# Optimization experiments

Hardware: AMD Instinct MI355X
Metric: run time of the kernel (lower is better)

The kernel has to match this reference:

```python
import jax, jax.numpy as jnp
import numpy as np

SEQ_LEN = 4096
D_MODEL = 1024
OUT_DIM = 1024
KERNEL = 256
STRIDE = 16
NUM_HEADS = 16


def _p(key, *shape):
    return jax.random.normal(key, shape, dtype=jnp.float32) * 0.02


def setup_inputs() -> dict:
    key = jax.random.key(0)
    ks = jax.random.split(key, 12)
    return {
        "path": jax.random.normal(ks[0], (SEQ_LEN, D_MODEL), dtype=jnp.float32),
        # sliding_module (nn.MultiheadAttention, embed_dim=D_MODEL)
        "w_in1": _p(ks[1], 3 * D_MODEL, D_MODEL),
        "b_in1": jnp.zeros((3 * D_MODEL,), jnp.float32),
        "w_out1": _p(ks[2], D_MODEL, D_MODEL),
        "b_out1": jnp.zeros((D_MODEL,), jnp.float32),
        # linear_module
        "w_lin": _p(ks[3], OUT_DIM, D_MODEL),
        "b_lin": jnp.zeros((OUT_DIM,), jnp.float32),
        # accum_module (embed_dim=OUT_DIM)
        "w_in2": _p(ks[4], 3 * OUT_DIM, OUT_DIM),
        "b_in2": jnp.zeros((3 * OUT_DIM,), jnp.float32),
        "w_out2": _p(ks[5], OUT_DIM, OUT_DIM),
        "b_out2": jnp.zeros((OUT_DIM,), jnp.float32),
    }


def _mha(q, k, v, w_in, b_in, w_out, b_out, num_heads):
    """torch nn.MultiheadAttention math (dropout=0). q,k,v: [..., L, E]."""
    E = q.shape[-1]
    Dh = E // num_heads
    wq, wk, wv = jnp.split(w_in, 3, axis=0)
    bq, bk, bv = jnp.split(b_in, 3)
    def heads(t):
        return t.reshape(t.shape[:-1] + (num_heads, Dh))
    qh = heads(q @ wq.T + bq)
    kh = heads(k @ wk.T + bk)
    vh = heads(v @ wv.T + bv)
    scale = 1.0 / np.sqrt(Dh).astype(np.float32)
    att = jax.nn.softmax(jnp.einsum("...qhd,...khd->...hqk", qh, kh) * scale, axis=-1)
    out = jnp.einsum("...hqk,...khd->...qhd", att, vh)
    out = out.reshape(out.shape[:-2] + (E,))
    return out @ w_out.T + b_out


def reference(path, w_in1, b_in1, w_out1, b_out1, w_lin, b_lin,
              w_in2, b_in2, w_out2, b_out2):
    seq_len = path.shape[-2]
    slices_num = (seq_len - KERNEL) // STRIDE
    # overlapping windows: [slices_num, KERNEL, D_MODEL]
    idx = jnp.arange(slices_num)[:, None] * STRIDE + jnp.arange(KERNEL)[None, :]
    x = path[idx]
    # batched self-attention over windows
    x = _mha(x, x, x, w_in1, b_in1, w_out1, b_out1, NUM_HEADS)
    x = jax.nn.relu(x @ w_lin.T + b_lin)  # [slices_num, KERNEL, OUT_DIM]
    # sequential recurrent attention accumulation
    def step(cum_att, xi):
        new = _mha(xi, cum_att, cum_att, w_in2, b_in2, w_out2, b_out2, NUM_HEADS)
        return new, None
    cum_att, _ = jax.lax.scan(step, x[0], x[1:])
    return cum_att  # [KERNEL, OUT_DIM]
```

## Files before the change

kernel.cpp:

```cpp
#include <hip/hip_runtime.h>
#include <math.h>

#define D_MODEL 1024
#define N_WIN   240
#define TOK     256
#define NH      16
#define DH      64
#define CHUNK   8
#define NCHUNK  30
#define WIN     ((size_t)TOK * D_MODEL)

typedef unsigned short ushort_t;
typedef unsigned long long ull_t;
typedef __attribute__((ext_vector_type(8))) short short8;
typedef __attribute__((ext_vector_type(4))) float floatx4;

__device__ __forceinline__ ushort_t f2bf(float f) {
    unsigned u = __float_as_uint(f);
    unsigned lsb = (u >> 16) & 1u;
    u += 0x7fffu + lsb;
    return (ushort_t)(u >> 16);
}

__device__ __forceinline__ void st2_wt(ushort_t* p, ushort_t v) {
    unsigned vv = v;
    asm volatile("global_store_short %0, %1, off sc1"
                 :: "v"(p), "v"(vv) : "memory");
}
__device__ __forceinline__ void st8_wt(ushort_t* p, ushort4 v) {
    ull_t dv = (ull_t)((unsigned)v.x | ((unsigned)v.y << 16))
             | ((ull_t)((unsigned)v.z | ((unsigned)v.w << 16)) << 32);
    asm volatile("global_store_dwordx2 %0, %1, off sc1"
                 :: "v"(p), "v"(dv) : "memory");
}
__device__ __forceinline__ void rel_drain() {
    asm volatile("s_waitcnt vmcnt(0)" ::: "memory");
}

#define GLDS(g, l) __builtin_amdgcn_global_load_lds( \
    (const __attribute__((address_space(1))) unsigned int*)(g), \
    (__attribute__((address_space(3))) unsigned int*)(l), 16, 0, 0)

__device__ __forceinline__ void grid_bar(unsigned* base, int g, unsigned s)
{
    rel_drain();
    __syncthreads();
    if (threadIdx.x == 0) {
        unsigned old = __hip_atomic_fetch_add(base + g * 32, 1u,
                __ATOMIC_RELAXED, __HIP_MEMORY_SCOPE_AGENT);
        if (old == 8u * s - 1u) {
            unsigned r = __hip_atomic_fetch_add(base + 256, 1u,
                    __ATOMIC_RELAXED, __HIP_MEMORY_SCOPE_AGENT);
            if (r == 8u * s - 1u)
                __hip_atomic_store(base + 288, s, __ATOMIC_RELAXED,
                                   __HIP_MEMORY_SCOPE_AGENT);
        }
        while (__hip_atomic_load(base + 288, __ATOMIC_RELAXED,
                                 __HIP_MEMORY_SCOPE_AGENT) < s)
            __builtin_amdgcn_s_sleep(1);
    }
    __syncthreads();
}

__device__ __forceinline__ void help_bar(unsigned* base, int g, unsigned s)
{
    rel_drain();
    __syncthreads();
    if (threadIdx.x == 0) {
        unsigned old = __hip_atomic_fetch_add(base + 1024 + g * 32, 1u,
                __ATOMIC_RELAXED, __HIP_MEMORY_SCOPE_AGENT);
        if (old == 8u * s - 1u) {
            unsigned r = __hip_atomic_fetch_add(base + 1800, 1u,
                    __ATOMIC_RELAXED, __HIP_MEMORY_SCOPE_AGENT);
            if (r == 24u * s - 1u)
                __hip_atomic_store(base + 1832, s, __ATOMIC_RELAXED,
                                   __HIP_MEMORY_SCOPE_AGENT);
        }
        while (__hip_atomic_load(base + 1832, __ATOMIC_RELAXED,
                                 __HIP_MEMORY_SCOPE_AGENT) < s)
            __builtin_amdgcn_s_sleep(1);
    }
    __syncthreads();
}

__global__ __launch_bounds__(256) void cast_bf_k(
    const float* __restrict__ s, ushort_t* __restrict__ d, int n)
{
    int i = (blockIdx.x * 256 + threadIdx.x) * 4;
    if (i >= n) return;
    float4 v = *(const float4*)(s + i);
    ushort4 o;
    o.x = f2bf(v.x); o.y = f2bf(v.y); o.z = f2bf(v.z); o.w = f2bf(v.w);
    *(ushort4*)(d + i) = o;
}

__global__ __launch_bounds__(256) void transpose_k(
    const ushort_t* __restrict__ src, ushort_t* __restrict__ dst)
{
    __shared__ ushort_t t[64][65];
    const int bx = blockIdx.x * 64, by = blockIdx.y * 64;
    const int c = threadIdx.x & 63, r0 = threadIdx.x >> 6;
#pragma unroll
    for (int k = 0; k < 16; ++k) {
        int r = r0 + k * 4;
        t[r][c] = src[(size_t)(by + r) * 1024 + bx + c];
    }
    __syncthreads();
#pragma unroll
    for (int k = 0; k < 16; ++k) {
        int r = r0 + k * 4;
        dst[(size_t)(bx + r) * 1024 + by + c] = t[c][r];
    }
}

__global__ __launch_bounds__(256) void bc_k(
    const float* __restrict__ w_in2, const float* __restrict__ b_in2,
    const float* __restrict__ b_out2, float* __restrict__ bc)
{
    int n = blockIdx.x * 256 + threadIdx.x;
    const float* row = w_in2 + (size_t)(1024 + n) * 1024;
    float s = b_in2[1024 + n];
    for (int j = 0; j < 1024; j += 4) {
        float4 w = *(const float4*)(row + j);
        float4 b = *(const float4*)(b_out2 + j);
        s += w.x * b.x + w.y * b.y + w.z * b.z + w.w * b.w;
    }
    bc[n] = s;
}

template<bool GATHER, bool WT>
__device__ __forceinline__ void gemm_core(
    ushort_t* As, ushort_t* Bs,
    const ushort_t* __restrict__ A, int lda, int w0,
    const ushort_t* __restrict__ W, const float* __restrict__ bias,
    ushort_t* __restrict__ Cb, float* __restrict__ Cf, int ldc,
    int K, int m0, int n0, int co, int relu)
{
    const int tid = threadIdx.x;
    const int wave = tid >> 6, lane = tid & 63;
    const int wm = wave & 1, wn = wave >> 1;

    int r0 = m0 + (tid >> 2), r1 = r0 + 64;
    if (GATHER) {
        r0 = (w0 + (r0 >> 8)) * 16 + (r0 & 255);
        r1 = (w0 + (r1 >> 8)) * 16 + (r1 & 255);
    }
    const int kcol = (tid & 3) * 8;
    const ushort_t* gA0 = A + (size_t)r0 * lda + kcol;
    const ushort_t* gA1 = A + (size_t)r1 * lda + kcol;
    const ushort_t* pW  = W + (size_t)n0 * K;
    const ushort_t* gB0 = pW + (size_t)(tid >> 2) * K + kcol;
    const ushort_t* gB1 = gB0 + (size_t)64 * K;
    ushort_t* lA = As + wave * 512;
    ushort_t* lB = Bs + wave * 512;

    floatx4 acc[4][4];
#pragma unroll
    for (int i = 0; i < 4; ++i)
#pragma unroll
        for (int j = 0; j < 4; ++j) acc[i][j] = (floatx4){0.f, 0.f, 0.f, 0.f};

    const int fr = lane & 15, fk = (lane >> 4) * 8;
    const int arow = (wm * 64 + fr) * 32 + fk;
    const int brow = (wn * 64 + fr) * 32 + fk;

    for (int k0 = 0; k0 < K; k0 += 32) {
        GLDS(gA0 + k0, lA);
        GLDS(gA1 + k0, lA + 2048);
        GLDS(gB0 + k0, lB);
        GLDS(gB1 + k0, lB + 2048);
        __syncthreads();
        short8 a[4], b[4];
#pragma unroll
        for (int mi = 0; mi < 4; ++mi) a[mi] = *(const short8*)&As[arow + mi * 512];
#pragma unroll
        for (int ni = 0; ni < 4; ++ni) b[ni] = *(const short8*)&Bs[brow + ni * 512];
#pragma unroll
        for (int mi = 0; mi < 4; ++mi)
#pragma unroll
            for (int ni = 0; ni < 4; ++ni)
                acc[mi][ni] = __builtin_amdgcn_mfma_f32_16x16x32_bf16(
                    a[mi], b[ni], acc[mi][ni], 0, 0, 0);
        __syncthreads();
    }

    const int crq = (lane >> 4) * 4;
    const int ccol = lane & 15;
#pragma unroll
    for (int mi = 0; mi < 4; ++mi) {
#pragma unroll
        for (int ni = 0; ni < 4; ++ni) {
            int lc = wn * 64 + ni * 16 + ccol;
            float bz = bias[n0 + lc];
#pragma unroll
            for (int rg = 0; rg < 4; ++rg) {
                int row = m0 + wm * 64 + mi * 16 + crq + rg;
                float v = acc[mi][ni][rg] + bz;
                if (relu) v = fmaxf(v, 0.f);
                size_t off = (size_t)row * ldc + co + lc;
                if (Cb) {
                    if (WT) st2_wt(Cb + off, f2bf(v));
                    else    Cb[off] = f2bf(v);
                }
                if (Cf) Cf[off] = v;
            }
        }
    }
}

__global__ __launch_bounds__(256) void gemm_bf_k(
    const ushort_t* __restrict__ A, int lda,
    const ushort_t* __restrict__ W, const float* __restrict__ bias,
    ushort_t* __restrict__ Cb, float* __restrict__ Cf, int ldc,
    int K, int relu)
{
    __shared__ ushort_t As[128 * 32];
    __shared__ ushort_t Bs[128 * 32];
    gemm_core<false, false>(As, Bs, A, lda, 0, W, bias, Cb, Cf, ldc, K,
                            blockIdx.y * 128, blockIdx.x * 128, blockIdx.x * 128, relu);
}

__global__ __launch_bounds__(256) void gemm_qkv_k(
    const ushort_t* __restrict__ path_bf, const ushort_t* __restrict__ W,
    const float* __restrict__ bias, ushort_t* __restrict__ Cb, int w0)
{
    __shared__ ushort_t As[128 * 32];
    __shared__ ushort_t Bs[128 * 32];
    gemm_core<true, false>(As, Bs, path_bf, 1024, w0, W, bias, Cb, nullptr, 3072, 1024,
                           blockIdx.y * 128, blockIdx.x * 128, blockIdx.x * 128, 0);
}

#define PLD 260
#define VLD 132

struct AttnShared {
    ushort_t P[64 * PLD];
    ushort_t VT[64 * VLD];
    float    l[64];
};

__device__ void attn_body(AttnShared& sh,
    const ushort_t* __restrict__ qkv, ushort_t* __restrict__ ao,
    int rs, int h, int b)
{
    const ushort_t* base = qkv + (size_t)b * TOK * 3072;
    const ushort_t* Q = base;
    const ushort_t* K = base + 1024;
    const ushort_t* V = base + 2048;
    ushort_t* O = ao + (size_t)b * TOK * 1024;
    const int ldq = 3072, ldkv = 3072, ldo = 1024;
    const int tid = threadIdx.x;
    const int wave = tid >> 6, lane = tid & 63;
    const int fr = lane & 15, q = lane >> 4, fk = q * 8;
    const ushort_t* Qh = Q + (size_t)(rs * 64) * ldq + h * 64;
    const ushort_t* Kh = K + h * 64;
    const ushort_t* Vh = V + h * 64;
    const int m0 = wave * 16;

    floatx4 s[16];
#pragma unroll
    for (int nt = 0; nt < 16; ++nt) s[nt] = (floatx4){0.f, 0.f, 0.f, 0.f};
#pragma unroll
    for (int kc = 0; kc < 64; kc += 32) {
        short8 a = *(const short8*)(Qh + (size_t)(m0 + fr) * ldq + kc + fk);
#pragma unroll
        for (int nt = 0; nt < 16; ++nt) {
            short8 b2 = *(const short8*)(Kh + (size_t)(nt * 16 + fr) * ldkv + kc + fk);
            s[nt] = __builtin_amdgcn_mfma_f32_16x16x32_bf16(a, b2, s[nt], 0, 0, 0);
        }
    }

    float rmax[4] = {-INFINITY, -INFINITY, -INFINITY, -INFINITY};
#pragma unroll
    for (int nt = 0; nt < 16; ++nt)
#pragma unroll
        for (int rg = 0; rg < 4; ++rg) rmax[rg] = fmaxf(rmax[rg], s[nt][rg]);
#pragma unroll
    for (int d = 1; d < 16; d <<= 1)
#pragma unroll
        for (int rg = 0; rg < 4; ++rg)
            rmax[rg] = fmaxf(rmax[rg], __shfl_xor(rmax[rg], d));

    float rsum[4] = {0.f, 0.f, 0.f, 0.f};
#pragma unroll
    for (int nt = 0; nt < 16; ++nt) {
#pragma unroll
        for (int rg = 0; rg < 4; ++rg) {
            float p = __expf((s[nt][rg] - rmax[rg]) * 0.125f);
            rsum[rg] += p;
            sh.P[(m0 + q * 4 + rg) * PLD + nt * 16 + fr] = f2bf(p);
        }
    }
#pragma unroll
    for (int d = 1; d < 16; d <<= 1)
#pragma unroll
        for (int rg = 0; rg < 4; ++rg) rsum[rg] += __shfl_xor(rsum[rg], d);
    if (fr == 0) {
#pragma unroll
        for (int rg = 0; rg < 4; ++rg) sh.l[m0 + q * 4 + rg] = rsum[rg];
    }
    __syncthreads();

    floatx4 o[4];
#pragma unroll
    for (int i = 0; i < 4; ++i) o[i] = (floatx4){0.f, 0.f, 0.f, 0.f};

#pragma unroll
    for (int half = 0; half < 2; ++half) {
        {
            int r = tid & 127, cp = tid >> 7;
            const ushort_t* vrow = Vh + (size_t)(half * 128 + r) * ldkv + cp * 32;
#pragma unroll
            for (int c = 0; c < 4; ++c) {
                uint4 pk = *(const uint4*)(vrow + c * 8);
                int d0 = cp * 32 + c * 8;
                sh.VT[(d0 + 0) * VLD + r] = (ushort_t)(pk.x & 0xffff);
                sh.VT[(d0 + 1) * VLD + r] = (ushort_t)(pk.x >> 16);
                sh.VT[(d0 + 2) * VLD + r] = (ushort_t)(pk.y & 0xffff);
                sh.VT[(d0 + 3) * VLD + r] = (ushort_t)(pk.y >> 16);
                sh.VT[(d0 + 4) * VLD + r] = (ushort_t)(pk.z & 0xffff);
                sh.VT[(d0 + 5) * VLD + r] = (ushort_t)(pk.z >> 16);
                sh.VT[(d0 + 6) * VLD + r] = (ushort_t)(pk.w & 0xffff);
                sh.VT[(d0 + 7) * VLD + r] = (ushort_t)(pk.w >> 16);
            }
        }
        __syncthreads();
#pragma unroll
        for (int ks = 0; ks < 4; ++ks) {
            short8 a = *(const short8*)&sh.P[(m0 + fr) * PLD + half * 128 + ks * 32 + fk];
#pragma unroll
            for (int nt2 = 0; nt2 < 4; ++nt2) {
                short8 b2 = *(const short8*)&sh.VT[(nt2 * 16 + fr) * VLD + ks * 32 + fk];
                o[nt2] = __builtin_amdgcn_mfma_f32_16x16x32_bf16(a, b2, o[nt2], 0, 0, 0);
            }
        }
        __syncthreads();
    }

    float linv[4];
#pragma unroll
    for (int rg = 0; rg < 4; ++rg) linv[rg] = 1.f / sh.l[m0 + q * 4 + rg];
#pragma unroll
    for (int nt2 = 0; nt2 < 4; ++nt2)
#pragma unroll
        for (int rg = 0; rg < 4; ++rg) {
            int row = rs * 64 + m0 + q * 4 + rg;
            st2_wt(O + (size_t)row * ldo + h * 64 + nt2 * 16 + fr,
                   f2bf(o[nt2][rg] * linv[rg]));
        }
    __syncthreads();
}

__global__ __launch_bounds__(256) void attn_mfma_k(
    const ushort_t* __restrict__ qkv, ushort_t* __restrict__ ao)
{
    __shared__ AttnShared sh;
    attn_body(sh, qkv, ao, blockIdx.x, blockIdx.y, blockIdx.z);
}

#define KLD 76
#define TLD 264

struct ScanSmem {
    union {
        struct { ushort_t Ab[2][4096]; ushort_t Wb[3][8192]; } st;
        struct { ushort_t Kl[256 * KLD]; ushort_t Vt[64 * TLD];
                 ushort_t P[64 * TLD]; } at;
    };
};

__device__ __forceinline__ void stage_A(
    const ushort_t* __restrict__ A64, int k0, ushort_t* __restrict__ Ad,
    int wave, int lane)
{
#pragma unroll
    for (int t = 0; t < 2; ++t) {
        int j = wave * 128 + t * 64 + lane;
        int row = j >> 3;
        int blk = (j & 7) ^ (row & 7);
        GLDS(A64 + (size_t)row * 1024 + k0 + blk * 8,
             Ad + wave * 1024 + t * 512);
    }
}

__device__ __forceinline__ void stage_W(
    const ushort_t* __restrict__ Wsel, int h, int k0,
    ushort_t* __restrict__ Wd, int wave, int lane)
{
#pragma unroll
    for (int t = 0; t < 4; ++t) {
        int j = wave * 256 + t * 64 + lane;
        int r = j >> 3;
        int blk = (j & 7) ^ (r & 7);
        int n = ((r >> 6) << 10) + h * 64 + (r & 63);
        GLDS(Wsel + (size_t)n * 1024 + k0 + blk * 8,
             Wd + wave * 2048 + t * 512);
    }
}

__device__ void scan_body(
    ScanSmem& sm, int h, int rs, int g,
    const ushort_t* __restrict__ Qchunk, int i0, int w0, int nsteps,
    const ushort_t* __restrict__ x0, ushort_t* __restrict__ AOb,
    ushort_t* __restrict__ KVx,
    const ushort_t* __restrict__ Wkv, const float* __restrict__ bkv,
    const ushort_t* __restrict__ Wc, const float* __restrict__ bc,
    unsigned* __restrict__ bar, unsigned s0)
{
    const int tid = threadIdx.x;
    const int wave = tid >> 6, lane = tid & 63;
    const int fr = lane & 15, q = lane >> 4, fk = q * 8;
    const int m0g = rs * 64 + wave * 16;

    const int dbofs = (wave < 2 ? 0 : 1024) + h * 64 + (wave & 1) * 32;
    float bK1[2], bC1[2];
#pragma unroll
    for (int nt = 0; nt < 2; ++nt) {
        bK1[nt] = bkv[dbofs + nt * 16 + fr];
        bC1[nt] = bc[dbofs + nt * 16 + fr];
    }

    ushort_t* Kl = sm.at.Kl;
    ushort_t* Vt = sm.at.Vt;
    ushort_t* P  = sm.at.P;

    short8 qf0, qf1;
    {
        const int i = i0;
        const ushort_t* Wsel0 = (i == 1) ? Wkv : Wc;
        stage_W(Wsel0, h, 0,  sm.st.Wb[0], wave, lane);
        stage_W(Wsel0, h, 64, sm.st.Wb[1], wave, lane);
        const ushort_t* Qrow = Qchunk + (size_t)(i - w0) * WIN
            + (size_t)(m0g + fr) * 1024 + h * 64;
        qf0 = *(const short8*)(Qrow);
        qf1 = *(const short8*)(Qrow + 32);
        const ushort_t* Asrc0 = (i == 1) ? x0
            : AOb + (size_t)((i - 1) & 7) * WIN;
        stage_A(Asrc0 + (size_t)rs * 64 * 1024, 0, sm.st.Ab[0], wave, lane);
    }

    unsigned s = s0;
    for (int t0 = 0; t0 < nsteps; ++t0, ++s) {
        const int i = i0 + t0;
        const ushort_t* Asrc = (i == 1) ? x0
            : AOb + (size_t)((i - 1) & 7) * WIN;
        const ushort_t* Wsel = (i == 1) ? Wkv : Wc;
        const ushort_t* A64 = Asrc + (size_t)rs * 64 * 1024;
        ushort_t* KVs = KVx + (size_t)(i & 7) * (NH * 32768) + h * 32768;

        floatx4 acc[4][2];
#pragma unroll
        for (int mt = 0; mt < 4; ++mt)
#pragma unroll
            for (int nt = 0; nt < 2; ++nt)
                acc[mt][nt] = (floatx4){0.f, 0.f, 0.f, 0.f};

#pragma unroll 1
        for (int t = 0; t < 16; ++t) {
            if (t < 15)
                stage_A(A64, (t + 1) * 64, sm.st.Ab[(t + 1) & 1], wave, lane);
            if (t < 14)
                stage_W(Wsel, h, (t + 2) * 64, sm.st.Wb[(t + 2) % 3], wave, lane);
            if (t == 15)
                asm volatile("s_waitcnt vmcnt(0)" ::: "memory");
            else if (t == 0 || t == 14)
                asm volatile("s_waitcnt vmcnt(6)" ::: "memory");
            else
                asm volatile("s_waitcnt vmcnt(10)" ::: "memory");
            __builtin_amdgcn_s_barrier();
            const ushort_t* Ac  = sm.st.Ab[t & 1];
            const ushort_t* Wc_ = sm.st.Wb[t % 3];
#pragma unroll
            for (int kh = 0; kh < 2; ++kh) {
                const int pb = (((kh << 2) + q) ^ (fr & 7)) * 8;
                short8 a[4];
#pragma unroll
                for (int mt = 0; mt < 4; ++mt)
                    a[mt] = *(const short8*)&Ac[(mt * 16 + fr) * 64 + pb];
#pragma unroll
                for (int nt = 0; nt < 2; ++nt) {
                    short8 b = *(const short8*)
                        &Wc_[(wave * 32 + nt * 16 + fr) * 64 + pb];
#pragma unroll
                    for (int mt = 0; mt < 4; ++mt)
                        acc[mt][nt] = __builtin_amdgcn_mfma_f32_16x16x32_bf16(
                            a[mt], b, acc[mt][nt], 0, 0, 0);
                }
            }
            asm volatile("s_waitcnt lgkmcnt(0)" ::: "memory");
            __builtin_amdgcn_sched_barrier(0);
            __builtin_amdgcn_s_barrier();
        }

        ushort_t* Kx = KVs;
        ushort_t* Vx = KVs + 16384;
#pragma unroll
        for (int mt = 0; mt < 4; ++mt) {
#pragma unroll
            for (int nt = 0; nt < 2; ++nt) {
                const float bz = (i == 1) ? bK1[nt] : bC1[nt];
                const int d = (wave & 1) * 32 + nt * 16 + fr;
                if (wave < 2) {
#pragma unroll
                    for (int rg = 0; rg < 4; ++rg) {
                        const int key = rs * 64 + mt * 16 + q * 4 + rg;
                        st2_wt(Kx + key * 64 + d, f2bf(acc[mt][nt][rg] + bz));
                    }
                } else {
                    ushort4 pv;
                    pv.x = f2bf(acc[mt][nt][0] + bz);
                    pv.y = f2bf(acc[mt][nt][1] + bz);
                    pv.z = f2bf(acc[mt][nt][2] + bz);
                    pv.w = f2bf(acc[mt][nt][3] + bz);
                    st8_wt(Vx + d * 256 + rs * 64 + mt * 16 + q * 4, pv);
                }
            }
        }
        rel_drain();
        __syncthreads();
        if (tid == 0)
            __hip_atomic_fetch_add(bar + 384 + h * 32, 1u,
                    __ATOMIC_RELAXED, __HIP_MEMORY_SCOPE_AGENT);

#pragma unroll
        for (int mt = 0; mt < 4; ++mt) {
#pragma unroll
            for (int nt = 0; nt < 2; ++nt) {
                const float bz = (i == 1) ? bK1[nt] : bC1[nt];
                const int d = (wave & 1) * 32 + nt * 16 + fr;
                if (wave < 2) {
#pragma unroll
                    for (int rg = 0; rg < 4; ++rg) {
                        const int key = rs * 64 + mt * 16 + q * 4 + rg;
                        Kl[key * KLD + d] = f2bf(acc[mt][nt][rg] + bz);
                    }
                } else {
                    ushort4 pv;
                    pv.x = f2bf(acc[mt][nt][0] + bz);
                    pv.y = f2bf(acc[mt][nt][1] + bz);
                    pv.z = f2bf(acc[mt][nt][2] + bz);
                    pv.w = f2bf(acc[mt][nt][3] + bz);
                    *(ushort4*)&Vt[d * TLD + rs * 64 + mt * 16 + q * 4] = pv;
                }
            }
        }
        if (tid == 0) {
            while (__hip_atomic_load(bar + 384 + h * 32, __ATOMIC_RELAXED,
                                     __HIP_MEMORY_SCOPE_AGENT) < 4u * s)
                __builtin_amdgcn_s_sleep(1);
        }
        __syncthreads();

        {
            if (wave != rs) {
                const ushort_t* kr = Kx + tid * 64;
                uint4 kb4[8];
#pragma unroll
                for (int s8 = 0; s8 < 8; ++s8)
                    kb4[s8] = *(const uint4*)(kr + s8 * 8);
                const int kp = (tid >> 4) & 3;
#pragma unroll
                for (int s8 = 0; s8 < 8; ++s8) {
                    int ks = (s8 + kp) & 7;
                    *(uint4*)&Kl[tid * KLD + ks * 8] = kb4[ks];
                }
            }
            const int vd = tid >> 2, vq = tid & 3;
            if (vq != rs) {
                const ushort_t* vr = Vx + vd * 256 + vq * 64;
                uint4 vb4[8];
#pragma unroll
                for (int s8 = 0; s8 < 8; ++s8)
                    vb4[s8] = *(const uint4*)(vr + s8 * 8);
                const int vp = vq << 1;
#pragma unroll
                for (int s8 = 0; s8 < 8; ++s8) {
                    int vs = (s8 + vp) & 7;
                    *(uint4*)&Vt[vd * TLD + vq * 64 + vs * 8] = vb4[vs];
                }
            }
        }
        __syncthreads();

        ushort_t* AOcur = AOb + (size_t)(i & 7) * WIN;
        {
            const int pl0 = wave * 16;
            floatx4 sc[16];
#pragma unroll
            for (int nt = 0; nt < 16; ++nt) sc[nt] = (floatx4){0.f, 0.f, 0.f, 0.f};
#pragma unroll
            for (int kc = 0; kc < 64; kc += 32) {
                short8 a = (kc == 0) ? qf0 : qf1;
#pragma unroll
                for (int nt = 0; nt < 16; ++nt) {
                    short8 b = *(const short8*)&Kl[(nt * 16 + fr) * KLD + kc + fk];
                    sc[nt] = __builtin_amdgcn_mfma_f32_16x16x32_bf16(
                        a, b, sc[nt], 0, 0, 0);
                }
            }
            float rmax[4] = {-INFINITY, -INFINITY, -INFINITY, -INFINITY};
#pragma unroll
            for (int nt = 0; nt < 16; ++nt)
#pragma unroll
                for (int rg = 0; rg < 4; ++rg) rmax[rg] = fmaxf(rmax[rg], sc[nt][rg]);
#pragma unroll
            for (int d = 1; d < 16; d <<= 1)
#pragma unroll
                for (int rg = 0; rg < 4; ++rg)
                    rmax[rg] = fmaxf(rmax[rg], __shfl_xor(rmax[rg], d));
            float rsum[4] = {0.f, 0.f, 0.f, 0.f};
#pragma unroll
            for (int nt = 0; nt < 16; ++nt) {
#pragma unroll
                for (int rg = 0; rg < 4; ++rg) {
                    float p = __expf((sc[nt][rg] - rmax[rg]) * 0.125f);
                    rsum[rg] += p;
                    P[(pl0 + q * 4 + rg) * TLD + nt * 16 + fr] = f2bf(p);
                }
            }
#pragma unroll
            for (int d = 1; d < 16; d <<= 1)
#pragma unroll
                for (int rg = 0; rg < 4; ++rg) rsum[rg] += __shfl_xor(rsum[rg], d);

            floatx4 o[4];
#pragma unroll
            for (int nt = 0; nt < 4; ++nt) o[nt] = (floatx4){0.f, 0.f, 0.f, 0.f};
#pragma unroll
            for (int kt = 0; kt < 8; ++kt) {
                short8 a = *(const short8*)&P[(pl0 + fr) * TLD + kt * 32 + fk];
#pragma unroll
                for (int nt = 0; nt < 4; ++nt) {
                    short8 b = *(const short8*)&Vt[(nt * 16 + fr) * TLD + kt * 32 + fk];
                    o[nt] = __builtin_amdgcn_mfma_f32_16x16x32_bf16(
                        a, b, o[nt], 0, 0, 0);
                }
            }
            float linv[4];
#pragma unroll
            for (int rg = 0; rg < 4; ++rg) linv[rg] = 1.f / rsum[rg];
#pragma unroll
            for (int nt = 0; nt < 4; ++nt)
#pragma unroll
                for (int rg = 0; rg < 4; ++rg) {
                    int row = m0g + q * 4 + rg;
                    st2_wt(AOcur + (size_t)row * 1024 + h * 64 + nt * 16 + fr,
                           f2bf(o[nt][rg] * linv[rg]));
                }
        }

        rel_drain();
        __syncthreads();
        if (tid == 0) {
            unsigned old = __hip_atomic_fetch_add(bar + g * 32, 1u,
                    __ATOMIC_RELAXED, __HIP_MEMORY_SCOPE_AGENT);
            if (old == 8u * s - 1u) {
                unsigned r = __hip_atomic_fetch_add(bar + 256, 1u,
                        __ATOMIC_RELAXED, __HIP_MEMORY_SCOPE_AGENT);
                if (r == 8u * s - 1u)
                    __hip_atomic_store(bar + 288, s, __ATOMIC_RELAXED,
                                       __HIP_MEMORY_SCOPE_AGENT);
            }
        }
        const bool more = (t0 + 1 < nsteps);
        if (more) {
            stage_W(Wc, h, 0,  sm.st.Wb[0], wave, lane);
            stage_W(Wc, h, 64, sm.st.Wb[1], wave, lane);
            const ushort_t* Qrow = Qchunk + (size_t)(i + 1 - w0) * WIN
                + (size_t)(m0g + fr) * 1024 + h * 64;
            qf0 = *(const short8*)(Qrow);
            qf1 = *(const short8*)(Qrow + 32);
        }
        if (tid == 0) {
            while (__hip_atomic_load(bar + 288, __ATOMIC_RELAXED,
                                     __HIP_MEMORY_SCOPE_AGENT) < s)
                __builtin_amdgcn_s_sleep(1);
        }
        __syncthreads();
        if (more)
            stage_A(AOb + (size_t)(i & 7) * WIN + (size_t)rs * 64 * 1024, 0,
                    sm.st.Ab[0], wave, lane);
    }
}

struct GemmSmem { ushort_t As[128 * 32]; ushort_t Bs[128 * 32]; };
union FusedSmem { ScanSmem scan; GemmSmem gem; AttnShared att; };

__global__ __launch_bounds__(256, 1) void fused_k(
    const ushort_t* __restrict__ Qchunk, int i0, int w0, int nsteps,
    const ushort_t* __restrict__ x0, ushort_t* __restrict__ AOb,
    ushort_t* __restrict__ KVx,
    const ushort_t* __restrict__ Wkv, const float* __restrict__ bkv,
    const ushort_t* __restrict__ Wc, const float* __restrict__ bc,
    unsigned* __restrict__ bar, unsigned s0,
    int do_help, int w0n,
    const ushort_t* __restrict__ path_bf,
    const ushort_t* __restrict__ w_in1, const float* __restrict__ b_in1,
    ushort_t* __restrict__ qkv, ushort_t* __restrict__ ao,
    ushort_t* __restrict__ ybuf,
    const ushort_t* __restrict__ w_out1, const float* __restrict__ b_out1,
    const ushort_t* __restrict__ w_lin, const float* __restrict__ b_lin,
    ushort_t* __restrict__ Xc,
    const ushort_t* __restrict__ w_in2, const float* __restrict__ b_in2,
    ushort_t* __restrict__ Qnext, unsigned hs0)
{
    __shared__ FusedSmem sm;
    const int wg = blockIdx.x;
    const int x = wg & 7, y = wg >> 3;

    if (x < 2) {
        const int scanIdx = x * 32 + y;
        const int h  = (x << 3) | (y >> 2);
        const int rs = y & 3;
        const int g  = scanIdx & 7;
        scan_body(sm.scan, h, rs, g,
                  Qchunk, i0, w0, nsteps, x0, AOb, KVx,
                  Wkv, bkv, Wc, bc, bar, s0);
        return;
    }
    if (!do_help) return;

    const int hw = (x - 2) * 32 + y;
    const int hg = hw >> 3;

    for (int t = hw; t < 384; t += 192) {
        int bx = t % 24, by = t / 24;
        gemm_core<true, true>(sm.gem.As, sm.gem.Bs, path_bf, 1024, w0n,
                              w_in1, b_in1, qkv, nullptr, 3072, 1024,
                              by * 128, bx * 128, bx * 128, 0);
    }
    help_bar(bar, hg, hs0);

    for (int t = hw; t < 512; t += 192) {
        int rs = t & 3, h = (t >> 2) & 15, b = t >> 6;
        attn_body(sm.att, qkv, ao, rs, h, b);
    }
    help_bar(bar, hg, hs0 + 1);

    for (int t = hw; t < 128; t += 192) {
        int bx = t & 7, by = t >> 3;
        gemm_core<false, true>(sm.gem.As, sm.gem.Bs, ao, 1024, 0,
                               w_out1, b_out1, ybuf, nullptr, 1024, 1024,
                               by * 128, bx * 128, bx * 128, 0);
    }
    help_bar(bar, hg, hs0 + 2);

    for (int t = hw; t < 128; t += 192) {
        int bx = t & 7, by = t >> 3;
        gemm_core<false, true>(sm.gem.As, sm.gem.Bs, ybuf, 1024, 0,
                               w_lin, b_lin, Xc, nullptr, 1024, 1024,
                               by * 128, bx * 128, bx * 128, 1);
    }
    help_bar(bar, hg, hs0 + 3);

    for (int t = hw; t < 128; t += 192) {
        int bx = t & 7, by = t >> 3;
        gemm_core<false, true>(sm.gem.As, sm.gem.Bs, Xc, 1024, 0,
                               w_in2, b_in2, Qnext, nullptr, 1024, 1024,
                               by * 128, bx * 128, bx * 128, 0);
    }
}

extern "C" void kernel_launch(void* const* d_in, const int* in_sizes, int n_in,
                              void* d_out, int out_size, void* d_ws, size_t ws_size,
                              hipStream_t stream)
{
    const float* path   = (const float*)d_in[0];
    const float* w_in1  = (const float*)d_in[1];
    const float* b_in1  = (const float*)d_in[2];
    const float* w_out1 = (const float*)d_in[3];
    const float* b_out1 = (const float*)d_in[4];
    const float* w_lin  = (const float*)d_in[5];
    const float* b_lin  = (const float*)d_in[6];
    const float* w_in2  = (const float*)d_in[7];
    const float* b_in2  = (const float*)d_in[8];
    const float* w_out2 = (const float*)d_in[9];
    const float* b_out2 = (const float*)d_in[10];
    float* out = (float*)d_out;

    unsigned* bar = (unsigned*)d_ws;
    float* bc      = (float*)d_ws + 2048;
    float* zerosf  = bc + 2048;
    ushort_t* ws = (ushort_t*)d_ws + 16384;
    ushort_t* path_bf  = ws;
    ushort_t* w_in1_bf = path_bf  + (size_t)4096 * 1024;
    ushort_t* w_out1_bf= w_in1_bf + (size_t)3072 * 1024;
    ushort_t* w_lin_bf = w_out1_bf+ (size_t)1024 * 1024;
    ushort_t* w_in2_bf = w_lin_bf + (size_t)1024 * 1024;
    ushort_t* w_out2_bf= w_in2_bf + (size_t)3072 * 1024;
    ushort_t* WoT_bf   = w_out2_bf+ (size_t)1024 * 1024;
    ushort_t* Wc_bf    = WoT_bf   + (size_t)1024 * 1024;
    ushort_t* qkv_bf   = Wc_bf    + (size_t)2048 * 1024;
    ushort_t* ao_bf    = qkv_bf   + (size_t)2048 * 3072;
    ushort_t* ybuf_bf  = ao_bf    + (size_t)2048 * 1024;
    ushort_t* Xbuf     = ybuf_bf  + (size_t)2048 * 1024;
    ushort_t* Qb0      = Xbuf     + (size_t)2048 * 1024;
    ushort_t* Qb1      = Qb0      + (size_t)2048 * 1024;
    ushort_t* AOb      = Qb1      + (size_t)2048 * 1024;
    ushort_t* x0buf    = AOb + 8 * WIN;
    ushort_t* dummy    = x0buf + WIN;
    ushort_t* KVx      = dummy + WIN;
    ushort_t* Qb[2] = {Qb0, Qb1};

    hipMemsetAsync(bar, 0, 8192, stream);
    hipMemsetAsync(zerosf, 0, 1024 * sizeof(float), stream);

    cast_bf_k<<<4096, 256, 0, stream>>>(path,  path_bf,  4096 * 1024);
    cast_bf_k<<<3072, 256, 0, stream>>>(w_in1, w_in1_bf, 3072 * 1024);
    cast_bf_k<<<1024, 256, 0, stream>>>(w_out1, w_out1_bf, 1024 * 1024);
    cast_bf_k<<<1024, 256, 0, stream>>>(w_lin, w_lin_bf, 1024 * 1024);
    cast_bf_k<<<3072, 256, 0, stream>>>(w_in2, w_in2_bf, 3072 * 1024);
    cast_bf_k<<<1024, 256, 0, stream>>>(w_out2, w_out2_bf, 1024 * 1024);

    transpose_k<<<dim3(16, 16), 256, 0, stream>>>(w_out2_bf, WoT_bf);
    bc_k<<<8, 256, 0, stream>>>(w_in2, b_in2, b_out2, bc);
    gemm_bf_k<<<dim3(8, 16), 256, 0, stream>>>(
        w_in2_bf + (size_t)1024 * 1024, 1024, WoT_bf, zerosf,
        Wc_bf, nullptr, 1024, 1024, 0);

    gemm_qkv_k<<<dim3(24, 16), 256, 0, stream>>>(
        path_bf, w_in1_bf, b_in1, qkv_bf, 0);
    attn_mfma_k<<<dim3(4, NH, CHUNK), 256, 0, stream>>>(qkv_bf, ao_bf);
    gemm_bf_k<<<dim3(8, 16), 256, 0, stream>>>(
        ao_bf, 1024, w_out1_bf, b_out1, ybuf_bf, nullptr, 1024, 1024, 0);
    gemm_bf_k<<<dim3(8, 16), 256, 0, stream>>>(
        ybuf_bf, 1024, w_lin_bf, b_lin, Xbuf, nullptr, 1024, 1024, 1);
    gemm_bf_k<<<dim3(8, 16), 256, 0, stream>>>(
        Xbuf, 1024, w_in2_bf, b_in2, Qb[0], nullptr, 1024, 1024, 0);
    (void)hipMemcpyAsync(x0buf, Xbuf, WIN * sizeof(ushort_t),
                         hipMemcpyDeviceToDevice, stream);

    unsigned sbase = 1;
    for (int c = 0; c < NCHUNK; ++c) {
        int w0 = c * CHUNK;
        int i0 = (c == 0) ? 1 : w0;
        int nsteps = (c == 0) ? CHUNK - 1 : CHUNK;
        int do_help = (c + 1 < NCHUNK) ? 1 : 0;
        int w0n = (c + 1) * CHUNK;
        unsigned hs0 = (unsigned)(c * 4 + 1);
        const ushort_t* Qcur = Qb[c & 1];
        ushort_t* Qnext = Qb[(c + 1) & 1];
        const ushort_t* x0P = x0buf;
        ushort_t* AObP = AOb;
        ushort_t* KVxP = KVx;
        const ushort_t* WkvP = w_in2_bf + (size_t)1024 * 1024;
        const float* bkvP = b_in2 + 1024;
        const ushort_t* WcP = Wc_bf;
        const float* bcP = bc;
        unsigned* barP = bar;
        unsigned sb = sbase;
        const ushort_t* pathP = path_bf;
        const ushort_t* win1P = w_in1_bf;
        const float* bin1P = b_in1;
        ushort_t* qkvP = qkv_bf;
        ushort_t* aoP = ao_bf;
        ushort_t* ybufP = ybuf_bf;
        const ushort_t* wout1P = w_out1_bf;
        const float* bout1P = b_out1;
        const ushort_t* wlinP = w_lin_bf;
        const float* blinP = b_lin;
        ushort_t* XP = Xbuf;
        const ushort_t* win2P = w_in2_bf;
        const float* bin2P = b_in2;
        void* args[] = {&Qcur, &i0, &w0, &nsteps, &x0P, &AObP, &KVxP,
                        &WkvP, &bkvP, &WcP, &bcP, &barP, &sb,
                        &do_help, &w0n, &pathP, &win1P, &bin1P,
                        &qkvP, &aoP, &ybufP, &wout1P, &bout1P,
                        &wlinP, &blinP, &XP, &win2P, &bin2P, &Qnext, &hs0};
        hipLaunchCooperativeKernel((void*)fused_k, dim3(256), dim3(256),
                                   args, 0, stream);
        sbase += (unsigned)nsteps;
    }

    gemm_bf_k<<<dim3(8, 2), 256, 0, stream>>>(
        AOb + (size_t)((N_WIN - 1) & 7) * WIN, 1024, w_out2_bf, b_out2,
        dummy, out, 1024, 1024, 0);
}
```

Baseline: 6.434 ms.

## Deepen LDS staging buffers and drop per-k-step trailing barrier in scan GEMM

The scan projection GEMM now uses three A buffers and four W buffers in shared memory instead of two and three. With the extra buffer, the staging for step t no longer overwrites data still being read, so the second s_barrier and the lgkmcnt drain at the end of each k-step are removed, leaving one barrier per step. The vmcnt wait is also set uniformly to 6. Separately, the spin-wait on the grid barrier is skipped on the final scan step, and an unused grid_bar helper is deleted. The cost is more LDS use, and the rotating buffer indexing must stay free of races.

```diff
diff --git a/kernel.cpp b/kernel.cpp
--- a/kernel.cpp
+++ b/kernel.cpp
@@ -40,27 +40,6 @@
 #define GLDS(g, l) __builtin_amdgcn_global_load_lds( \
     (const __attribute__((address_space(1))) unsigned int*)(g), \
     (__attribute__((address_space(3))) unsigned int*)(l), 16, 0, 0)
-
-__device__ __forceinline__ void grid_bar(unsigned* base, int g, unsigned s)
-{
-    rel_drain();
-    __syncthreads();
-    if (threadIdx.x == 0) {
-        unsigned old = __hip_atomic_fetch_add(base + g * 32, 1u,
-                __ATOMIC_RELAXED, __HIP_MEMORY_SCOPE_AGENT);
-        if (old == 8u * s - 1u) {
-            unsigned r = __hip_atomic_fetch_add(base + 256, 1u,
-                    __ATOMIC_RELAXED, __HIP_MEMORY_SCOPE_AGENT);
-            if (r == 8u * s - 1u)
-                __hip_atomic_store(base + 288, s, __ATOMIC_RELAXED,
-                                   __HIP_MEMORY_SCOPE_AGENT);
-        }
-        while (__hip_atomic_load(base + 288, __ATOMIC_RELAXED,
-                                 __HIP_MEMORY_SCOPE_AGENT) < s)
-            __builtin_amdgcn_s_sleep(1);
-    }
-    __syncthreads();
-}
 
 __device__ __forceinline__ void help_bar(unsigned* base, int g, unsigned s)
 {
@@ -363,7 +342,7 @@
 
 struct ScanSmem {
     union {
-        struct { ushort_t Ab[2][4096]; ushort_t Wb[3][8192]; } st;
+        struct { ushort_t Ab[3][4096]; ushort_t Wb[4][8192]; } st;
         struct { ushort_t Kl[256 * KLD]; ushort_t Vt[64 * TLD];
                  ushort_t P[64 * TLD]; } at;
     };
@@ -458,18 +437,16 @@
 #pragma unroll 1
         for (int t = 0; t < 16; ++t) {
             if (t < 15)
-                stage_A(A64, (t + 1) * 64, sm.st.Ab[(t + 1) & 1], wave, lane);
+                stage_A(A64, (t + 1) * 64, sm.st.Ab[(t + 1) % 3], wave, lane);
             if (t < 14)
-                stage_W(Wsel, h, (t + 2) * 64, sm.st.Wb[(t + 2) % 3], wave, lane);
+                stage_W(Wsel, h, (t + 2) * 64, sm.st.Wb[(t + 2) & 3], wave, lane);
             if (t == 15)
                 asm volatile("s_waitcnt vmcnt(0)" ::: "memory");
-            else if (t == 0 || t == 14)
+            else
                 asm volatile("s_waitcnt vmcnt(6)" ::: "memory");
-            else
-                asm volatile("s_waitcnt vmcnt(10)" ::: "memory");
             __builtin_amdgcn_s_barrier();
-            const ushort_t* Ac  = sm.st.Ab[t & 1];
-            const ushort_t* Wc_ = sm.st.Wb[t % 3];
+            const ushort_t* Ac  = sm.st.Ab[t % 3];
+            const ushort_t* Wc_ = sm.st.Wb[t & 3];
 #pragma unroll
             for (int kh = 0; kh < 2; ++kh) {
                 const int pb = (((kh << 2) + q) ^ (fr & 7)) * 8;
@@ -487,11 +464,8 @@
                             a[mt], b, acc[mt][nt], 0, 0, 0);
                 }
             }
-            asm volatile("s_waitcnt lgkmcnt(0)" ::: "memory");
-            __builtin_amdgcn_sched_barrier(0);
-            __builtin_amdgcn_s_barrier();
-        }
-
+        }
+        __builtin_amdgcn_s_barrier();
         ushort_t* Kx = KVs;
         ushort_t* Vx = KVs + 16384;
 #pragma unroll
@@ -671,7 +645,7 @@
             qf0 = *(const short8*)(Qrow);
             qf1 = *(const short8*)(Qrow + 32);
         }
-        if (tid == 0) {
+        if (tid == 0 && more) {
             while (__hip_atomic_load(bar + 288, __ATOMIC_RELAXED,
                                      __HIP_MEMORY_SCOPE_AGENT) < s)
                 __builtin_amdgcn_s_sleep(1);
```

Result: faster. 6.207 ms (-3.5%).
